# Optimization experiments

Measured on AMD Instinct MI355X. Metric: run time of the kernel, lower is better.

Reference implementation:

```python
import jax, jax.numpy as jnp
import numpy as np

TEMPERATURE = 0.1
NUM_CLASSES = 32
BATCH = 8192
HIDDEN = 256


def setup_inputs() -> dict:
    key = jax.random.key(0)
    k1, k2 = jax.random.split(key)
    features = jax.random.normal(k1, (BATCH, HIDDEN), dtype=jnp.float32)
    labels = jax.random.randint(k2, (BATCH,), 0, NUM_CLASSES)
    return {"features": features, "labels": labels}


def reference(features, labels):
    B = features.shape[0]
    # L2 normalize rows, pairwise cosine sim scaled by temperature
    f = features / jnp.linalg.norm(features, axis=1, keepdims=True)
    sim = (f @ f.T) / TEMPERATURE                       # [B, B]
    offdiag = 1.0 - jnp.eye(B, dtype=sim.dtype)
    E = jnp.exp(sim) * offdiag                          # exp sims, self excluded

    onehot = (labels[:, None] == jnp.arange(NUM_CLASSES)[None, :]).astype(sim.dtype)  # [B, C]
    # per-anchor, per-class sum of exp-sims (excluding self)
    class_sum = E @ onehot                              # [B, C]
    # per-anchor class counts excluding self
    counts = onehot.sum(0)[None, :] - onehot            # [B, C]
    # denominator_i = sum over classes with members (excluding i) of class mean
    denom = jnp.where(counts > 0, class_sum / jnp.maximum(counts, 1.0), 0.0).sum(axis=1)  # [B]

    # positives: same label, not self
    pos_mask = (onehot @ onehot.T) * offdiag            # [B, B]
    P = pos_mask.sum(axis=1)                            # number of positives per anchor
    valid = P > 0
    # -mean_p log(exp(sim[i,p]) / denom_i) = log(denom_i) - mean_p sim[i,p]
    mean_pos_sim = (sim * pos_mask).sum(axis=1) / jnp.maximum(P, 1.0)
    loss_i = jnp.where(valid, jnp.log(jnp.maximum(denom, 1e-30)) - mean_pos_sim, 0.0)

    n_valid = valid.sum()
    loss = jnp.where(n_valid > 0, loss_i.sum() / jnp.maximum(n_valid, 1).astype(sim.dtype), 0.0)
    return loss
```

## Files before the change

kernel.cpp:

```cpp
#include <hip/hip_runtime.h>
#include <hip/hip_bf16.h>
#include <math.h>
#include <string.h>

#define B_SZ  8192
#define KD    256
#define NCLS  32
#define NCHUNK 8
#define JTPC   8
#define SCALE_LOG2 3.79828243f
#define LN2 0.69314718056f

typedef __attribute__((ext_vector_type(8))) short short8;
typedef __attribute__((ext_vector_type(4))) float f32x4;

static __device__ __forceinline__ unsigned pk2bf(float a, float b) {
    __hip_bfloat162 h = __float22bfloat162_rn(make_float2(a, b));
    unsigned u; __builtin_memcpy(&u, &h, 4); return u;
}
static __device__ __forceinline__ unsigned short f2bf1(float f) {
    unsigned u = __float_as_uint(f);
    return (unsigned short)((u + 0x7FFF + ((u >> 16) & 1)) >> 16);
}
static __device__ __forceinline__ float fexp2(float x) {
    float r;
    asm("v_exp_f32 %0, %1" : "=v"(r) : "v"(x));
    return r;
}

__global__ void prep_kernel(const float* __restrict__ feat, unsigned short* __restrict__ Fbf) {
    int row  = blockIdx.x * 4 + (threadIdx.x >> 6);
    int lane = threadIdx.x & 63;
    const float4 v = ((const float4*)(feat + (size_t)row * KD))[lane];
    float s = v.x * v.x + v.y * v.y + v.z * v.z + v.w * v.w;
    #pragma unroll
    for (int off = 1; off < 64; off <<= 1) s += __shfl_xor(s, off, 64);
    float rn = rsqrtf(s) * SCALE_LOG2;
    uint2 w;
    w.x = pk2bf(v.x * rn, v.y * rn);
    w.y = pk2bf(v.z * rn, v.w * rn);
    ((uint2*)(Fbf + (size_t)row * KD))[lane] = w;
}

__global__ void count_kernel(const int* __restrict__ labels, int* __restrict__ counts) {
    __shared__ int sc[NCLS];
    int t = threadIdx.x;
    if (t < NCLS) sc[t] = 0;
    __syncthreads();
    for (int i = t; i < B_SZ; i += 256) atomicAdd(&sc[labels[i]], 1);
    __syncthreads();
    if (t < NCLS) counts[t] = sc[t];
}

__global__ __launch_bounds__(256, 2) void sim_kernel(
    const unsigned short* __restrict__ Fbf, const int* __restrict__ labels,
    unsigned short* __restrict__ pcls, float* __restrict__ ppos)
{
    __shared__ __align__(16) unsigned short sbuf[2][2][128 * 64];
    __shared__ int   slab[2][128];
    __shared__ float sps[128];

    const int bid = blockIdx.x;
    const int swz = (bid & 7) * 64 + (bid >> 3);
    const int itile = swz >> 3;
    const int jc    = swz & 7;
    const int i0    = itile * 128;

    const int t    = threadIdx.x;
    const int wave = t >> 6;
    const int lane = t & 63;
    const int wr   = wave >> 1;
    const int wc   = wave & 1;
    const int l15  = lane & 15;
    const int l4   = lane >> 4;

    int labi[4];
    #pragma unroll
    for (int m = 0; m < 4; m++) labi[m] = labels[i0 + wr * 64 + m * 16 + l15];

    const int rT = t >> 3;
    const int s8 = t & 7;

    auto STAGE = [&](int buf, int j0s, int ks) {
        const int kc = ks * 64;
        #pragma unroll
        for (int a = 0; a < 4; ++a) {
            int r   = a * 32 + rT;
            int sl  = s8 ^ (r & 7);
            int col = kc + sl * 8;
            const unsigned short* gA = Fbf + (size_t)(i0 + r) * KD + col;
            char* lA = (char*)&sbuf[buf][0][0] + a * 4096 + wave * 1024;
            __builtin_amdgcn_global_load_lds(
                (const __attribute__((address_space(1))) void*)gA,
                (__attribute__((address_space(3))) void*)lA, 16, 0, 0);
            const unsigned short* gB = Fbf + (size_t)(j0s + r) * KD + col;
            char* lB = (char*)&sbuf[buf][1][0] + a * 4096 + wave * 1024;
            __builtin_amdgcn_global_load_lds(
                (const __attribute__((address_space(1))) void*)gB,
                (__attribute__((address_space(3))) void*)lB, 16, 0, 0);
        }
    };

    f32x4 acc_cs[4][2];
    float psum[4] = {0.f, 0.f, 0.f, 0.f};
    #pragma unroll
    for (int m = 0; m < 4; m++)
        #pragma unroll
        for (int cb = 0; cb < 2; cb++)
            acc_cs[m][cb] = (f32x4){0.f, 0.f, 0.f, 0.f};

    const int jt_beg = jc * JTPC;
    const int rot = bid & 7;
    {
        const int jf0 = (jt_beg + rot) * 128;
        if (t < 128) slab[0][t] = labels[jf0 + t];
        STAGE(0, jf0, 0);
    }

    #pragma unroll 1
    for (int k = 0; k < JTPC; ++k) {
        const int jt = jt_beg + ((k + rot) & 7);
        const int j0 = jt * 128;
        const int cur = k & 1;

        __syncthreads();

        f32x4 acc[4][4];
        #pragma unroll
        for (int m = 0; m < 4; m++)
            #pragma unroll
            for (int n = 0; n < 4; n++)
                acc[m][n] = (f32x4){0.f, 0.f, 0.f, 0.f};

        #pragma unroll 1
        for (int ks = 0; ks < 4; ++ks) {
            if (ks < 3) STAGE((ks + 1) & 1, j0, ks + 1);
            const unsigned short* pA = &sbuf[ks & 1][0][0];
            const unsigned short* pB = &sbuf[ks & 1][1][0];
            short8 bf4[4][2];
            #pragma unroll
            for (int n = 0; n < 4; ++n) {
                int r = wc * 64 + n * 16 + l15;
                #pragma unroll
                for (int kk = 0; kk < 2; ++kk)
                    bf4[n][kk] = *(const short8*)&pB[r * 64 + (((kk * 4 + l4) ^ (r & 7)) * 8)];
            }
            __builtin_amdgcn_s_setprio(1);
            #pragma unroll
            for (int m = 0; m < 4; ++m) {
                int r = wr * 64 + m * 16 + l15;
                short8 a0 = *(const short8*)&pA[r * 64 + ((l4 ^ (r & 7)) * 8)];
                short8 a1 = *(const short8*)&pA[r * 64 + (((4 + l4) ^ (r & 7)) * 8)];
                #pragma unroll
                for (int n = 0; n < 4; ++n) {
                    acc[m][n] = __builtin_amdgcn_mfma_f32_16x16x32_bf16(bf4[n][0], a0, acc[m][n], 0, 0, 0);
                    acc[m][n] = __builtin_amdgcn_mfma_f32_16x16x32_bf16(bf4[n][1], a1, acc[m][n], 0, 0, 0);
                }
            }
            __builtin_amdgcn_s_setprio(0);
            __syncthreads();
        }

        if (k + 1 < JTPC) {
            const int jn0 = (jt_beg + ((k + 1 + rot) & 7)) * 128;
            STAGE(0, jn0, 0);
            if (t < 128) slab[cur ^ 1][t] = labels[jn0 + t];
        }

        char* sEw = (char*)&sbuf[1][0][0] + wave * 8192;

        int4 lj4[4];
        #pragma unroll
        for (int n = 0; n < 4; n++)
            lj4[n] = *(const int4*)&slab[cur][wc * 64 + n * 16 + l4 * 4];

        if (j0 != i0) {
            #pragma unroll
            for (int m = 0; m < 4; m++) {
                const int row = m * 16 + l15;
                #pragma unroll
                for (int n = 0; n < 4; n++) {
                    const int* ljp = (const int*)&lj4[n];
                    float e[4];
                    #pragma unroll
                    for (int q = 0; q < 4; q++) {
                        float sp = acc[m][n][q];
                        psum[m] += (ljp[q] == labi[m]) ? sp : 0.0f;
                        e[q] = fexp2(sp);
                    }
                    uint2 w; w.x = pk2bf(e[0], e[1]); w.y = pk2bf(e[2], e[3]);
                    const int bc = (n * 32 + l4 * 8) ^ ((row & 7) << 4);
                    *(uint2*)(sEw + row * 128 + bc) = w;
                }
            }
        } else {
            #pragma unroll
            for (int m = 0; m < 4; m++) {
                const int row = m * 16 + l15;
                const int ig = i0 + wr * 64 + row;
                #pragma unroll
                for (int n = 0; n < 4; n++) {
                    const int jb = wc * 64 + n * 16 + l4 * 4;
                    const int* ljp = (const int*)&lj4[n];
                    float e[4];
                    #pragma unroll
                    for (int q = 0; q < 4; q++) {
                        const int jg = j0 + jb + q;
                        float sp = acc[m][n][q];
                        bool self = (ig == jg);
                        psum[m] += (!self && ljp[q] == labi[m]) ? sp : 0.0f;
                        e[q] = self ? 0.0f : fexp2(sp);
                    }
                    uint2 w; w.x = pk2bf(e[0], e[1]); w.y = pk2bf(e[2], e[3]);
                    const int bc = (n * 32 + l4 * 8) ^ ((row & 7) << 4);
                    *(uint2*)(sEw + row * 128 + bc) = w;
                }
            }
        }

        short8 hf[2][2];
        #pragma unroll
        for (int kk = 0; kk < 2; kk++) {
            const int jb = wc * 64 + kk * 32 + l4 * 8;
            int4 lv0 = *(const int4*)&slab[cur][jb];
            int4 lv1 = *(const int4*)&slab[cur][jb + 4];
            int lv[8] = {lv0.x, lv0.y, lv0.z, lv0.w, lv1.x, lv1.y, lv1.z, lv1.w};
            #pragma unroll
            for (int cb = 0; cb < 2; cb++) {
                short8 h;
                #pragma unroll
                for (int e = 0; e < 8; e++)
                    h[e] = (lv[e] == cb * 16 + l15) ? (short)0x3F80 : (short)0;
                hf[kk][cb] = h;
            }
        }

        #pragma unroll
        for (int kk = 0; kk < 2; kk++) {
            #pragma unroll
            for (int m = 0; m < 4; m++) {
                const int row = m * 16 + l15;
                const int bc = (kk * 64 + l4 * 16) ^ ((row & 7) << 4);
                short8 ef = *(const short8*)(sEw + row * 128 + bc);
                #pragma unroll
                for (int cb = 0; cb < 2; cb++)
                    acc_cs[m][cb] = __builtin_amdgcn_mfma_f32_16x16x32_bf16(
                        ef, hf[kk][cb], acc_cs[m][cb], 0, 0, 0);
            }
        }
    }

    __syncthreads();
    float* scr = (float*)&sbuf[0][0][0];
    float pv[4];
    #pragma unroll
    for (int m = 0; m < 4; m++) {
        float v = psum[m];
        v += __shfl_xor(v, 16, 64);
        v += __shfl_xor(v, 32, 64);
        pv[m] = v;
    }
    if (wc == 1) {
        #pragma unroll
        for (int m = 0; m < 4; m++) {
            #pragma unroll
            for (int cb = 0; cb < 2; cb++)
                #pragma unroll
                for (int q = 0; q < 4; q++)
                    scr[(wr * 64 + m * 16 + l4 * 4 + q) * 33 + cb * 16 + l15] =
                        acc_cs[m][cb][q];
            if (l4 == 0) sps[wr * 64 + m * 16 + l15] = pv[m];
        }
    }
    __syncthreads();
    if (wc == 0) {
        const size_t slot = (size_t)itile * NCHUNK + jc;
        unsigned short* pc = pcls + slot * 128 * NCLS;
        #pragma unroll
        for (int m = 0; m < 4; m++) {
            #pragma unroll
            for (int cb = 0; cb < 2; cb++)
                #pragma unroll
                for (int q = 0; q < 4; q++) {
                    const int r = wr * 64 + m * 16 + l4 * 4 + q;
                    const int c = cb * 16 + l15;
                    pc[r * NCLS + c] = f2bf1(acc_cs[m][cb][q] + scr[r * 33 + c]);
                }
            if (l4 == 0)
                ppos[slot * 128 + wr * 64 + m * 16 + l15] =
                    (pv[m] + sps[wr * 64 + m * 16 + l15]) * LN2;
        }
    }
}

__global__ void reduce_kernel(const unsigned short* __restrict__ pcls, const float* __restrict__ ppos,
                              const int* __restrict__ counts, const int* __restrict__ labels,
                              float* __restrict__ loss_i, float* __restrict__ validf) {
    int tid = blockIdx.x * blockDim.x + threadIdx.x;
    int i  = tid >> 3;
    int cq = tid & 7;
    if (i >= B_SZ) return;
    int itile = i >> 7, ilocal = i & 127;

    f32x4 cs = (f32x4){0.f, 0.f, 0.f, 0.f};
    for (int ch = 0; ch < NCHUNK; ch++) {
        const unsigned short* p = pcls + ((size_t)(itile * NCHUNK + ch) * 128 + ilocal) * NCLS + cq * 4;
        ushort4 v = *(const ushort4*)p;
        const unsigned short* vp = (const unsigned short*)&v;
        #pragma unroll
        for (int e = 0; e < 4; e++)
            cs[e] += __uint_as_float((unsigned)vp[e] << 16);
    }
    int labi = labels[i];
    float dpart = 0.0f;
    #pragma unroll
    for (int e = 0; e < 4; e++) {
        int c = cq * 4 + e;
        int cnt = counts[c] - (c == labi ? 1 : 0);
        if (cnt > 0) dpart += cs[e] / (float)cnt;
    }
    #pragma unroll
    for (int off = 1; off < 8; off <<= 1) dpart += __shfl_xor(dpart, off, 64);

    if (cq == 0) {
        float psum = 0.0f;
        for (int ch = 0; ch < NCHUNK; ch++)
            psum += ppos[(size_t)(itile * NCHUNK + ch) * 128 + ilocal];
        int P = counts[labi] - 1;
        bool valid = P > 0;
        float li = 0.0f;
        if (valid) li = logf(fmaxf(dpart, 1e-30f)) - psum / (float)max(P, 1);
        loss_i[i] = li;
        validf[i] = valid ? 1.0f : 0.0f;
    }
}

__global__ void final_kernel(const float* __restrict__ loss_i, const float* __restrict__ validf,
                             float* __restrict__ out) {
    __shared__ float ssum[256];
    __shared__ float scnt[256];
    int t = threadIdx.x;
    float s = 0.0f, c = 0.0f;
    for (int i = t; i < B_SZ; i += 256) { s += loss_i[i]; c += validf[i]; }
    ssum[t] = s; scnt[t] = c;
    __syncthreads();
    #pragma unroll
    for (int off = 128; off > 0; off >>= 1) {
        if (t < off) { ssum[t] += ssum[t + off]; scnt[t] += scnt[t + off]; }
        __syncthreads();
    }
    if (t == 0) out[0] = (scnt[0] > 0.0f) ? ssum[0] / scnt[0] : 0.0f;
}

extern "C" void kernel_launch(void* const* d_in, const int* in_sizes, int n_in,
                              void* d_out, int out_size, void* d_ws, size_t ws_size,
                              hipStream_t stream) {
    const float* feat   = (const float*)d_in[0];
    const int*   labels = (const int*)d_in[1];
    float*       out    = (float*)d_out;

    char* ws = (char*)d_ws;
    size_t off = 0;
    auto alloc = [&](size_t bytes) -> void* {
        void* p = ws + off;
        off = (off + bytes + 255) & ~(size_t)255;
        return p;
    };

    unsigned short* Fbf = (unsigned short*)alloc((size_t)B_SZ * KD * 2);
    int*   counts = (int*)alloc((size_t)NCLS * 4);
    float* loss_i = (float*)alloc((size_t)B_SZ * 4);
    float* validf = (float*)alloc((size_t)B_SZ * 4);
    float* ppos   = (float*)alloc((size_t)512 * 128 * 4);
    unsigned short* pcls = (unsigned short*)alloc((size_t)512 * 128 * NCLS * 2);

    prep_kernel<<<B_SZ / 4, 256, 0, stream>>>(feat, Fbf);
    count_kernel<<<1, 256, 0, stream>>>(labels, counts);
    sim_kernel<<<512, 256, 0, stream>>>(Fbf, labels, pcls, ppos);
    reduce_kernel<<<B_SZ * 8 / 256, 256, 0, stream>>>(pcls, ppos, counts, labels, loss_i, validf);
    final_kernel<<<1, 256, 0, stream>>>(loss_i, validf, out);
}
```

Measured before the change: 85.01 us.

## Split sim_kernel tile across 8 waves and drop j-tile rotation

Doubles the sim_kernel block to 512 threads, so each wave covers 64x32 of the 128x128 tile instead of 64x64. This halves per-wave accumulators and MFMA work, aiming for more latency hiding and less register pressure. The class-sum partials from the three extra column waves are reduced through LDS at the end. It also removes the per-block rotation of j-tile order, so blocks sharing a chunk now read the same j tiles at the same time. That may contend on L2, and it costs a larger LDS scratch and a bigger reduction.

```diff
diff --git a/kernel.cpp b/kernel.cpp
--- a/kernel.cpp
+++ b/kernel.cpp
@@ -52,13 +52,13 @@
     if (t < NCLS) counts[t] = sc[t];
 }
 
-__global__ __launch_bounds__(256, 2) void sim_kernel(
+__global__ __launch_bounds__(512, 2) void sim_kernel(
     const unsigned short* __restrict__ Fbf, const int* __restrict__ labels,
     unsigned short* __restrict__ pcls, float* __restrict__ ppos)
 {
     __shared__ __align__(16) unsigned short sbuf[2][2][128 * 64];
     __shared__ int   slab[2][128];
-    __shared__ float sps[128];
+    __shared__ float sps[3][128];
 
     const int bid = blockIdx.x;
     const int swz = (bid & 7) * 64 + (bid >> 3);
@@ -69,8 +69,8 @@
     const int t    = threadIdx.x;
     const int wave = t >> 6;
     const int lane = t & 63;
-    const int wr   = wave >> 1;
-    const int wc   = wave & 1;
+    const int wr   = wave >> 2;
+    const int wc   = wave & 3;
     const int l15  = lane & 15;
     const int l4   = lane >> 4;
 
@@ -84,17 +84,17 @@
     auto STAGE = [&](int buf, int j0s, int ks) {
         const int kc = ks * 64;
         #pragma unroll
-        for (int a = 0; a < 4; ++a) {
-            int r   = a * 32 + rT;
+        for (int a = 0; a < 2; ++a) {
+            int r   = a * 64 + rT;
             int sl  = s8 ^ (r & 7);
             int col = kc + sl * 8;
             const unsigned short* gA = Fbf + (size_t)(i0 + r) * KD + col;
-            char* lA = (char*)&sbuf[buf][0][0] + a * 4096 + wave * 1024;
+            char* lA = (char*)&sbuf[buf][0][0] + a * 8192 + wave * 1024;
             __builtin_amdgcn_global_load_lds(
                 (const __attribute__((address_space(1))) void*)gA,
                 (__attribute__((address_space(3))) void*)lA, 16, 0, 0);
             const unsigned short* gB = Fbf + (size_t)(j0s + r) * KD + col;
-            char* lB = (char*)&sbuf[buf][1][0] + a * 4096 + wave * 1024;
+            char* lB = (char*)&sbuf[buf][1][0] + a * 8192 + wave * 1024;
             __builtin_amdgcn_global_load_lds(
                 (const __attribute__((address_space(1))) void*)gB,
                 (__attribute__((address_space(3))) void*)lB, 16, 0, 0);
@@ -109,27 +109,22 @@
         for (int cb = 0; cb < 2; cb++)
             acc_cs[m][cb] = (f32x4){0.f, 0.f, 0.f, 0.f};
 
-    const int jt_beg = jc * JTPC;
-    const int rot = bid & 7;
-    {
-        const int jf0 = (jt_beg + rot) * 128;
-        if (t < 128) slab[0][t] = labels[jf0 + t];
-        STAGE(0, jf0, 0);
-    }
+    const int jt_beg = jc * JTPC, jt_end = (jc + 1) * JTPC;
+    if (t < 128) slab[0][t] = labels[jt_beg * 128 + t];
+    STAGE(0, jt_beg * 128, 0);
 
     #pragma unroll 1
-    for (int k = 0; k < JTPC; ++k) {
-        const int jt = jt_beg + ((k + rot) & 7);
+    for (int jt = jt_beg; jt < jt_end; ++jt) {
         const int j0 = jt * 128;
-        const int cur = k & 1;
+        const int cur = jt & 1;
 
         __syncthreads();
 
-        f32x4 acc[4][4];
+        f32x4 acc[4][2];
         #pragma unroll
         for (int m = 0; m < 4; m++)
             #pragma unroll
-            for (int n = 0; n < 4; n++)
+            for (int n = 0; n < 2; n++)
                 acc[m][n] = (f32x4){0.f, 0.f, 0.f, 0.f};
 
         #pragma unroll 1
@@ -137,10 +132,10 @@
             if (ks < 3) STAGE((ks + 1) & 1, j0, ks + 1);
             const unsigned short* pA = &sbuf[ks & 1][0][0];
             const unsigned short* pB = &sbuf[ks & 1][1][0];
-            short8 bf4[4][2];
-            #pragma unroll
-            for (int n = 0; n < 4; ++n) {
-                int r = wc * 64 + n * 16 + l15;
+            short8 bf4[2][2];
+            #pragma unroll
+            for (int n = 0; n < 2; ++n) {
+                int r = wc * 32 + n * 16 + l15;
                 #pragma unroll
                 for (int kk = 0; kk < 2; ++kk)
                     bf4[n][kk] = *(const short8*)&pB[r * 64 + (((kk * 4 + l4) ^ (r & 7)) * 8)];
@@ -152,7 +147,7 @@
                 short8 a0 = *(const short8*)&pA[r * 64 + ((l4 ^ (r & 7)) * 8)];
                 short8 a1 = *(const short8*)&pA[r * 64 + (((4 + l4) ^ (r & 7)) * 8)];
                 #pragma unroll
-                for (int n = 0; n < 4; ++n) {
+                for (int n = 0; n < 2; ++n) {
                     acc[m][n] = __builtin_amdgcn_mfma_f32_16x16x32_bf16(bf4[n][0], a0, acc[m][n], 0, 0, 0);
                     acc[m][n] = __builtin_amdgcn_mfma_f32_16x16x32_bf16(bf4[n][1], a1, acc[m][n], 0, 0, 0);
                 }
@@ -161,25 +156,24 @@
             __syncthreads();
         }
 
-        if (k + 1 < JTPC) {
-            const int jn0 = (jt_beg + ((k + 1 + rot) & 7)) * 128;
-            STAGE(0, jn0, 0);
-            if (t < 128) slab[cur ^ 1][t] = labels[jn0 + t];
-        }
-
-        char* sEw = (char*)&sbuf[1][0][0] + wave * 8192;
-
-        int4 lj4[4];
-        #pragma unroll
-        for (int n = 0; n < 4; n++)
-            lj4[n] = *(const int4*)&slab[cur][wc * 64 + n * 16 + l4 * 4];
+        if (jt + 1 < jt_end) {
+            STAGE(0, (jt + 1) * 128, 0);
+            if (t < 128) slab[cur ^ 1][t] = labels[(jt + 1) * 128 + t];
+        }
+
+        char* sEw = (char*)&sbuf[1][0][0] + wave * 4096;
+
+        int4 lj4[2];
+        #pragma unroll
+        for (int n = 0; n < 2; n++)
+            lj4[n] = *(const int4*)&slab[cur][wc * 32 + n * 16 + l4 * 4];
 
         if (j0 != i0) {
             #pragma unroll
             for (int m = 0; m < 4; m++) {
                 const int row = m * 16 + l15;
                 #pragma unroll
-                for (int n = 0; n < 4; n++) {
+                for (int n = 0; n < 2; n++) {
                     const int* ljp = (const int*)&lj4[n];
                     float e[4];
                     #pragma unroll
@@ -189,8 +183,8 @@
                         e[q] = fexp2(sp);
                     }
                     uint2 w; w.x = pk2bf(e[0], e[1]); w.y = pk2bf(e[2], e[3]);
-                    const int bc = (n * 32 + l4 * 8) ^ ((row & 7) << 4);
-                    *(uint2*)(sEw + row * 128 + bc) = w;
+                    const int bc = (n * 32 + l4 * 8) ^ ((row & 3) << 4);
+                    *(uint2*)(sEw + row * 64 + bc) = w;
                 }
             }
         } else {
@@ -199,8 +193,8 @@
                 const int row = m * 16 + l15;
                 const int ig = i0 + wr * 64 + row;
                 #pragma unroll
-                for (int n = 0; n < 4; n++) {
-                    const int jb = wc * 64 + n * 16 + l4 * 4;
+                for (int n = 0; n < 2; n++) {
+                    const int jb = wc * 32 + n * 16 + l4 * 4;
                     const int* ljp = (const int*)&lj4[n];
                     float e[4];
                     #pragma unroll
@@ -212,16 +206,15 @@
                         e[q] = self ? 0.0f : fexp2(sp);
                     }
                     uint2 w; w.x = pk2bf(e[0], e[1]); w.y = pk2bf(e[2], e[3]);
-                    const int bc = (n * 32 + l4 * 8) ^ ((row & 7) << 4);
-                    *(uint2*)(sEw + row * 128 + bc) = w;
+                    const int bc = (n * 32 + l4 * 8) ^ ((row & 3) << 4);
+                    *(uint2*)(sEw + row * 64 + bc) = w;
                 }
             }
         }
 
-        short8 hf[2][2];
-        #pragma unroll
-        for (int kk = 0; kk < 2; kk++) {
-            const int jb = wc * 64 + kk * 32 + l4 * 8;
+        short8 hf[2];
+        {
+            const int jb = wc * 32 + l4 * 8;
             int4 lv0 = *(const int4*)&slab[cur][jb];
             int4 lv1 = *(const int4*)&slab[cur][jb + 4];
             int lv[8] = {lv0.x, lv0.y, lv0.z, lv0.w, lv1.x, lv1.y, lv1.z, lv1.w};
@@ -231,22 +224,19 @@
                 #pragma unroll
                 for (int e = 0; e < 8; e++)
                     h[e] = (lv[e] == cb * 16 + l15) ? (short)0x3F80 : (short)0;
-                hf[kk][cb] = h;
-            }
-        }
-
-        #pragma unroll
-        for (int kk = 0; kk < 2; kk++) {
-            #pragma unroll
-            for (int m = 0; m < 4; m++) {
-                const int row = m * 16 + l15;
-                const int bc = (kk * 64 + l4 * 16) ^ ((row & 7) << 4);
-                short8 ef = *(const short8*)(sEw + row * 128 + bc);
-                #pragma unroll
-                for (int cb = 0; cb < 2; cb++)
-                    acc_cs[m][cb] = __builtin_amdgcn_mfma_f32_16x16x32_bf16(
-                        ef, hf[kk][cb], acc_cs[m][cb], 0, 0, 0);
-            }
+                hf[cb] = h;
+            }
+        }
+
+        #pragma unroll
+        for (int m = 0; m < 4; m++) {
+            const int row = m * 16 + l15;
+            const int bc = (l4 * 16) ^ ((row & 3) << 4);
+            short8 ef = *(const short8*)(sEw + row * 64 + bc);
+            #pragma unroll
+            for (int cb = 0; cb < 2; cb++)
+                acc_cs[m][cb] = __builtin_amdgcn_mfma_f32_16x16x32_bf16(
+                    ef, hf[cb], acc_cs[m][cb], 0, 0, 0);
         }
     }
 
@@ -260,16 +250,17 @@
         v += __shfl_xor(v, 32, 64);
         pv[m] = v;
     }
-    if (wc == 1) {
+    if (wc > 0) {
+        const int k = wc - 1;
         #pragma unroll
         for (int m = 0; m < 4; m++) {
             #pragma unroll
             for (int cb = 0; cb < 2; cb++)
                 #pragma unroll
                 for (int q = 0; q < 4; q++)
-                    scr[(wr * 64 + m * 16 + l4 * 4 + q) * 33 + cb * 16 + l15] =
+                    scr[(size_t)k * 4224 + (wr * 64 + m * 16 + l4 * 4 + q) * 33 + cb * 16 + l15] =
                         acc_cs[m][cb][q];
-            if (l4 == 0) sps[wr * 64 + m * 16 + l15] = pv[m];
+            if (l4 == 0) sps[k][wr * 64 + m * 16 + l15] = pv[m];
         }
     }
     __syncthreads();
@@ -284,11 +275,16 @@
                 for (int q = 0; q < 4; q++) {
                     const int r = wr * 64 + m * 16 + l4 * 4 + q;
                     const int c = cb * 16 + l15;
-                    pc[r * NCLS + c] = f2bf1(acc_cs[m][cb][q] + scr[r * 33 + c]);
+                    float v = acc_cs[m][cb][q];
+                    #pragma unroll
+                    for (int k = 0; k < 3; k++) v += scr[(size_t)k * 4224 + r * 33 + c];
+                    pc[r * NCLS + c] = f2bf1(v);
                 }
-            if (l4 == 0)
-                ppos[slot * 128 + wr * 64 + m * 16 + l15] =
-                    (pv[m] + sps[wr * 64 + m * 16 + l15]) * LN2;
+            if (l4 == 0) {
+                const int r = wr * 64 + m * 16 + l15;
+                float v = pv[m] + sps[0][r] + sps[1][r] + sps[2][r];
+                ppos[slot * 128 + r] = v * LN2;
+            }
         }
     }
 }
@@ -376,7 +372,7 @@
 
     prep_kernel<<<B_SZ / 4, 256, 0, stream>>>(feat, Fbf);
     count_kernel<<<1, 256, 0, stream>>>(labels, counts);
-    sim_kernel<<<512, 256, 0, stream>>>(Fbf, labels, pcls, ppos);
+    sim_kernel<<<512, 512, 0, stream>>>(Fbf, labels, pcls, ppos);
     reduce_kernel<<<B_SZ * 8 / 256, 256, 0, stream>>>(pcls, ppos, counts, labels, loss_i, validf);
     final_kernel<<<1, 256, 0, stream>>>(loss_i, validf, out);
 }
```

Measured after the change: 111.0 us. 30.5% more time.
